# Optimization experiments

Hardware: AMD Instinct MI355X
Metric: run time of the kernel (lower is better)

The kernel has to match this reference:

```python
import jax, jax.numpy as jnp
import numpy as np

N, E = 40000, 640000
IN_DIM, EDGE_DIM, HID = 128, 64, 128


def setup_inputs() -> dict:
    key = jax.random.key(0)
    ks = jax.random.split(key, 10)
    x = jax.random.normal(ks[0], (N, IN_DIM), dtype=jnp.float32)
    edge_index = jax.random.randint(ks[1], (2, E), 0, N, dtype=jnp.int64)
    edge_attr = jax.random.normal(ks[2], (E, EDGE_DIM), dtype=jnp.float32)
    # learned params (xavier-ish scaling)
    Wh_w = jax.random.normal(ks[3], (EDGE_DIM, HID), dtype=jnp.float32) / np.sqrt(EDGE_DIM)
    Wh_b = jnp.zeros((HID,), dtype=jnp.float32)
    Wn_w = jax.random.normal(ks[4], (2 * IN_DIM, HID), dtype=jnp.float32) / np.sqrt(2 * IN_DIM)
    Wn_b = jnp.zeros((HID,), dtype=jnp.float32)
    w_e = jax.random.normal(ks[5], (HID, 1), dtype=jnp.float32) / np.sqrt(HID)
    ft_w = jax.random.normal(ks[6], (IN_DIM, IN_DIM), dtype=jnp.float32) / np.sqrt(IN_DIM)
    ft_b = jnp.zeros((IN_DIM,), dtype=jnp.float32)
    return {"x": x, "edge_index": edge_index, "edge_attr": edge_attr,
            "Wh_w": Wh_w, "Wh_b": Wh_b, "Wn_w": Wn_w, "Wn_b": Wn_b,
            "w_e": w_e, "ft_w": ft_w, "ft_b": ft_b}


def reference(x, edge_index, edge_attr, Wh_w, Wh_b, Wn_w, Wn_b, w_e, ft_w, ft_b):
    src, dst = edge_index[0], edge_index[1]
    # gather endpoint features and run edge MLP: relu(W_h(e) + W_n([x_src; x_dst]))
    node_feat = jnp.concatenate([x[src], x[dst]], axis=1)          # [E, 2*in_dim]
    edge_h = edge_attr @ Wh_w + Wh_b                               # [E, hid]
    node_h = node_feat @ Wn_w + Wn_b                               # [E, hid]
    combined = jax.nn.relu(edge_h + node_h)
    scores = (combined @ w_e)[:, 0]                                # [E]
    alpha = jax.nn.softmax(scores, axis=0)                         # softmax over all edges
    # scatter-add weighted dst features into src nodes (same-type branch)
    local = jnp.zeros_like(x).at[src].add(-alpha[:, None] * x[dst])
    out = x + local
    out = out + out @ ft_w + ft_b
    return out
```

## Files before the change

kernel.cpp:

```cpp
#include <hip/hip_runtime.h>
#include <math.h>

#define N_NODES 40000
#define E_EDGES 640000
#define IN_DIM 128
#define EDGE_DIM 64
#define HID 128
#define EB 10000
#define NPART (EB * 4)

typedef unsigned int u32;
typedef unsigned short u16;
typedef __attribute__((ext_vector_type(4))) float f32x4;
typedef __attribute__((ext_vector_type(8))) short bf16x8;

__device__ __forceinline__ float bf_lo(u32 d) { return __uint_as_float(d << 16); }
__device__ __forceinline__ float bf_hi(u32 d) { return __uint_as_float(d & 0xffff0000u); }
__device__ __forceinline__ u16 f2bf(float f) {
    u32 u = __float_as_uint(f);
    return (u16)((u + 0x7fffu + ((u >> 16) & 1u)) >> 16);
}
__device__ __forceinline__ u32 pack_bf(float lo, float hi) {
    return ((u32)f2bf(hi) << 16) | (u32)f2bf(lo);
}


__global__ __launch_bounds__(256) void k_init(const float* __restrict__ x,
                                              u16* __restrict__ xb,
                                              u32* __restrict__ counts) {
    int i = blockIdx.x * 256 + threadIdx.x;
    xb[i] = f2bf(x[i]);
    if (i < N_NODES) counts[i] = 0;
}

__global__ __launch_bounds__(256) void k_trans(const float* __restrict__ Whw,
                                               const float* __restrict__ Wnw,
                                               const float* __restrict__ ftw,
                                               u16* __restrict__ Whtb,
                                               u16* __restrict__ WnAT,
                                               u16* __restrict__ WnBT,
                                               u16* __restrict__ fttb) {
    int i = blockIdx.x * 256 + threadIdx.x;
    if (i < 8192) {
        int h = i >> 6, k = i & 63;
        Whtb[i] = f2bf(Whw[k * HID + h]);
    } else if (i < 24576) {
        int j = i - 8192, h = j >> 7, k = j & 127;
        WnAT[j] = f2bf(Wnw[k * HID + h]);
    } else if (i < 40960) {
        int j = i - 24576, h = j >> 7, k = j & 127;
        WnBT[j] = f2bf(Wnw[(IN_DIM + k) * HID + h]);
    } else {
        int j = i - 40960, h = j >> 7, k = j & 127;
        fttb[j] = f2bf(ftw[k * IN_DIM + h]);
    }
}

__global__ __launch_bounds__(256) void k_proj(const u16* __restrict__ xb,
                                              const u16* __restrict__ WnAT,
                                              const u16* __restrict__ WnBT,
                                              const float* __restrict__ Whb,
                                              const float* __restrict__ Wnb,
                                              u16* __restrict__ P1b,
                                              u16* __restrict__ P2b) {
    const int t = threadIdx.x, w = t >> 6, lane = t & 63;
    const int mrow = lane & 15, quad = lane >> 4;
    const int rowBase = blockIdx.x * 64 + w * 16;

    bf16x8 a[4];
    const u16* ar = xb + (size_t)(rowBase + mrow) * IN_DIM + quad * 8;
#pragma unroll
    for (int ks = 0; ks < 4; ++ks) a[ks] = *(const bf16x8*)(ar + ks * 32);

#pragma unroll
    for (int nt = 0; nt < 8; ++nt) {
        const u16* b1p = WnAT + (size_t)(nt * 16 + mrow) * IN_DIM + quad * 8;
        const u16* b2p = WnBT + (size_t)(nt * 16 + mrow) * IN_DIM + quad * 8;
        f32x4 c1 = {0.f, 0.f, 0.f, 0.f}, c2 = {0.f, 0.f, 0.f, 0.f};
#pragma unroll
        for (int ks = 0; ks < 4; ++ks) {
            c1 = __builtin_amdgcn_mfma_f32_16x16x32_bf16(a[ks], *(const bf16x8*)(b1p + ks * 32), c1, 0, 0, 0);
            c2 = __builtin_amdgcn_mfma_f32_16x16x32_bf16(a[ks], *(const bf16x8*)(b2p + ks * 32), c2, 0, 0, 0);
        }
        const int col = nt * 16 + mrow;
        const float bias = Whb[col] + Wnb[col];
#pragma unroll
        for (int r = 0; r < 4; ++r) {
            int row = rowBase + quad * 4 + r;
            P1b[(size_t)row * HID + col] = f2bf(c1[r] + bias);
            P2b[(size_t)row * HID + col] = f2bf(c2[r]);
        }
    }
}

__global__ __launch_bounds__(256) void k_hist(const int* __restrict__ eidx,
                                              u32* __restrict__ counts) {
    int e = blockIdx.x * 256 + threadIdx.x;
    atomicAdd(&counts[eidx[e]], 1u);
}

__global__ __launch_bounds__(1024) void k_scan(const u32* __restrict__ counts,
                                               u32* __restrict__ off,
                                               u32* __restrict__ cur) {
    __shared__ u32 sums[1024];
    const int t = threadIdx.x;
    const int CH = 40;
    u32 local[CH];
    u32 s = 0;
    const int base = t * CH;
#pragma unroll
    for (int i = 0; i < CH; ++i) {
        int idx = base + i;
        u32 c = (idx < N_NODES) ? counts[idx] : 0u;
        local[i] = s;
        s += c;
    }
    sums[t] = s;
    __syncthreads();
    for (int o = 1; o < 1024; o <<= 1) {
        u32 v = (t >= o) ? sums[t - o] : 0u;
        __syncthreads();
        sums[t] += v;
        __syncthreads();
    }
    const u32 pre = sums[t] - s;
#pragma unroll
    for (int i = 0; i < CH; ++i) {
        int idx = base + i;
        if (idx < N_NODES) {
            u32 v = pre + local[i];
            off[idx] = v;
            cur[idx] = v;
        }
    }
    if (t == 1023) off[N_NODES] = sums[1023];
}

__global__ __launch_bounds__(256) void k_edge(const int* __restrict__ eidx,
                                              const float* __restrict__ ea,
                                              const u16* __restrict__ Whtb,
                                              const u16* __restrict__ P1b,
                                              const u16* __restrict__ P2b,
                                              const float* __restrict__ we,
                                              u32* __restrict__ cur,
                                              uint2* __restrict__ sde,
                                              float* __restrict__ partials) {
    __shared__ u32 Psp[4][16][68];
    const int t = threadIdx.x, w = t >> 6, lane = t & 63;
    const int e0 = blockIdx.x * 64 + w * 16;
    const int mrow = lane & 15, quad = lane >> 4;

    const int m = lane >> 2, c4 = lane & 3;
    const int srcm = eidx[e0 + m];
    const int dstm = eidx[E_EDGES + e0 + m];
    const uint4* p1 = (const uint4*)(P1b + (size_t)srcm * HID + c4 * 32);
    const uint4* p2 = (const uint4*)(P2b + (size_t)dstm * HID + c4 * 32);
    uint4 pa[4], pb[4];
#pragma unroll
    for (int i = 0; i < 4; ++i) { pa[i] = p1[i]; pb[i] = p2[i]; }

    const float* arow = ea + (size_t)(e0 + mrow) * EDGE_DIM + quad * 8;
    float4 f0 = *(const float4*)(arow);
    float4 f1 = *(const float4*)(arow + 4);
    float4 f2 = *(const float4*)(arow + 32);
    float4 f3 = *(const float4*)(arow + 36);

#pragma unroll
    for (int i = 0; i < 4; ++i) {
        u32 da[4] = {pa[i].x, pa[i].y, pa[i].z, pa[i].w};
        u32 db[4] = {pb[i].x, pb[i].y, pb[i].z, pb[i].w};
        uint4 o;
        o.x = pack_bf(bf_lo(da[0]) + bf_lo(db[0]), bf_hi(da[0]) + bf_hi(db[0]));
        o.y = pack_bf(bf_lo(da[1]) + bf_lo(db[1]), bf_hi(da[1]) + bf_hi(db[1]));
        o.z = pack_bf(bf_lo(da[2]) + bf_lo(db[2]), bf_hi(da[2]) + bf_hi(db[2]));
        o.w = pack_bf(bf_lo(da[3]) + bf_lo(db[3]), bf_hi(da[3]) + bf_hi(db[3]));
        *(uint4*)&Psp[w][m][c4 * 16 + i * 4] = o;
    }

    bf16x8 a0, a1;
    a0[0] = (short)f2bf(f0.x); a0[1] = (short)f2bf(f0.y);
    a0[2] = (short)f2bf(f0.z); a0[3] = (short)f2bf(f0.w);
    a0[4] = (short)f2bf(f1.x); a0[5] = (short)f2bf(f1.y);
    a0[6] = (short)f2bf(f1.z); a0[7] = (short)f2bf(f1.w);
    a1[0] = (short)f2bf(f2.x); a1[1] = (short)f2bf(f2.y);
    a1[2] = (short)f2bf(f2.z); a1[3] = (short)f2bf(f2.w);
    a1[4] = (short)f2bf(f3.x); a1[5] = (short)f2bf(f3.y);
    a1[6] = (short)f2bf(f3.z); a1[7] = (short)f2bf(f3.w);

    float wsum[4] = {0.f, 0.f, 0.f, 0.f};
    const u16* bbase = Whtb + (size_t)mrow * EDGE_DIM + quad * 8;
#pragma unroll
    for (int nt = 0; nt < 8; ++nt) {
        const u16* bp = bbase + nt * 16 * EDGE_DIM;
        bf16x8 b0 = *(const bf16x8*)(bp);
        bf16x8 b1 = *(const bf16x8*)(bp + 32);
        f32x4 c = {0.f, 0.f, 0.f, 0.f};
        c = __builtin_amdgcn_mfma_f32_16x16x32_bf16(a0, b0, c, 0, 0, 0);
        c = __builtin_amdgcn_mfma_f32_16x16x32_bf16(a1, b1, c, 0, 0, 0);
        float wv = we[nt * 16 + mrow];
#pragma unroll
        for (int r = 0; r < 4; ++r) {
            u32 u = Psp[w][quad * 4 + r][nt * 8 + (mrow >> 1)];
            float p = (mrow & 1) ? bf_hi(u) : bf_lo(u);
            wsum[r] += fmaxf(c[r] + p, 0.f) * wv;
        }
    }

#pragma unroll
    for (int off = 1; off < 16; off <<= 1) {
#pragma unroll
        for (int r = 0; r < 4; ++r) wsum[r] += __shfl_xor(wsum[r], off, 16);
    }
    float ex[4]; float s4 = 0.f;
#pragma unroll
    for (int r = 0; r < 4; ++r) { ex[r] = __expf(wsum[r]); s4 += ex[r]; }

    if (mrow == 0) {
#pragma unroll
        for (int r = 0; r < 4; ++r) {
            int e = e0 + quad * 4 + r;
            int s = eidx[e];
            int d = eidx[E_EDGES + e];
            u32 pos = atomicAdd(&cur[s], 1u);
            sde[pos] = make_uint2((u32)d, __float_as_uint(-ex[r]));
        }
    }

    s4 += __shfl_xor(s4, 16, 64);
    s4 += __shfl_xor(s4, 32, 64);
    if (lane == 0) partials[blockIdx.x * 4 + w] = s4;
}

__global__ __launch_bounds__(256) void k_sum(const float* __restrict__ partials,
                                             float* __restrict__ sumExp) {
    float s = 0.f;
    for (int i = threadIdx.x; i < NPART; i += 256) s += partials[i];
#pragma unroll
    for (int off = 1; off < 64; off <<= 1) s += __shfl_xor(s, off, 64);
    __shared__ float ws4[4];
    if ((threadIdx.x & 63) == 0) ws4[threadIdx.x >> 6] = s;
    __syncthreads();
    if (threadIdx.x == 0) sumExp[0] = ws4[0] + ws4[1] + ws4[2] + ws4[3];
}

__global__ __launch_bounds__(256) void k_accum(const u32* __restrict__ off,
                                               const uint2* __restrict__ sde,
                                               const float* __restrict__ sumExp,
                                               const u16* __restrict__ xb,
                                               float* __restrict__ out) {
    const float invS = 1.0f / sumExp[0];
    const int lane = threadIdx.x & 63;
    const int n = blockIdx.x * 4 + (threadIdx.x >> 6);
    const u32 o0 = off[n], o1 = off[n + 1];

    float acc0 = 0.f, acc1 = 0.f;
    for (u32 base = o0; base < o1; base += 64) {
        u32 j = base + (u32)lane;
        uint2 dv = make_uint2(0u, 0u);
        if (j < o1) dv = sde[j];
        int cnt = (int)min(64u, o1 - base);
        int jj = 0;
        for (; jj + 4 <= cnt; jj += 4) {
            u32 d0 = __shfl(dv.x, jj, 64),     d1 = __shfl(dv.x, jj + 1, 64);
            u32 d2 = __shfl(dv.x, jj + 2, 64), d3 = __shfl(dv.x, jj + 3, 64);
            float a0 = __uint_as_float(__shfl(dv.y, jj, 64));
            float a1 = __uint_as_float(__shfl(dv.y, jj + 1, 64));
            float a2 = __uint_as_float(__shfl(dv.y, jj + 2, 64));
            float a3 = __uint_as_float(__shfl(dv.y, jj + 3, 64));
            u32 q0 = ((const u32*)(xb + (size_t)d0 * IN_DIM))[lane];
            u32 q1 = ((const u32*)(xb + (size_t)d1 * IN_DIM))[lane];
            u32 q2 = ((const u32*)(xb + (size_t)d2 * IN_DIM))[lane];
            u32 q3 = ((const u32*)(xb + (size_t)d3 * IN_DIM))[lane];
            acc0 = fmaf(a0, bf_lo(q0), acc0); acc1 = fmaf(a0, bf_hi(q0), acc1);
            acc0 = fmaf(a1, bf_lo(q1), acc0); acc1 = fmaf(a1, bf_hi(q1), acc1);
            acc0 = fmaf(a2, bf_lo(q2), acc0); acc1 = fmaf(a2, bf_hi(q2), acc1);
            acc0 = fmaf(a3, bf_lo(q3), acc0); acc1 = fmaf(a3, bf_hi(q3), acc1);
        }
        for (; jj < cnt; ++jj) {
            u32 dst = __shfl(dv.x, jj, 64);
            float a = __uint_as_float(__shfl(dv.y, jj, 64));
            u32 q = ((const u32*)(xb + (size_t)dst * IN_DIM))[lane];
            acc0 = fmaf(a, bf_lo(q), acc0);
            acc1 = fmaf(a, bf_hi(q), acc1);
        }
    }
    float* op = out + (size_t)n * IN_DIM + 2 * lane;
    op[0] = acc0 * invS;
    op[1] = acc1 * invS;
}

__global__ __launch_bounds__(256) void k_final(const float* __restrict__ x,
                                               const u16* __restrict__ fttb,
                                               const float* __restrict__ ftb,
                                               float* __restrict__ out) {
    __shared__ u32 ybp[64][68];
    const int t = threadIdx.x;
    const int rb = blockIdx.x * 64;

    {
        const int rr = t >> 2, seg = t & 3;
        const float4* xp = (const float4*)(x + (size_t)(rb + rr) * IN_DIM + seg * 32);
        const float4* lp = (const float4*)(out + (size_t)(rb + rr) * IN_DIM + seg * 32);
#pragma unroll
        for (int i = 0; i < 4; ++i) {
            float4 xa = xp[2 * i], xc = xp[2 * i + 1];
            float4 la = lp[2 * i], lc = lp[2 * i + 1];
            uint4 o;
            o.x = pack_bf(xa.x + la.x, xa.y + la.y);
            o.y = pack_bf(xa.z + la.z, xa.w + la.w);
            o.z = pack_bf(xc.x + lc.x, xc.y + lc.y);
            o.w = pack_bf(xc.z + lc.z, xc.w + lc.w);
            *(uint4*)&ybp[rr][seg * 16 + i * 4] = o;
        }
    }
    __syncthreads();

    const int w = t >> 6, lane = t & 63;
    const int mrow = lane & 15, quad = lane >> 4;
    const int rowBase = rb + w * 16;

    bf16x8 a[4];
#pragma unroll
    for (int ks = 0; ks < 4; ++ks)
        a[ks] = *(const bf16x8*)&ybp[w * 16 + mrow][ks * 16 + quad * 4];

#pragma unroll
    for (int nt = 0; nt < 8; ++nt) {
        const u16* bp = fttb + (size_t)(nt * 16 + mrow) * IN_DIM + quad * 8;
        f32x4 c = {0.f, 0.f, 0.f, 0.f};
#pragma unroll
        for (int ks = 0; ks < 4; ++ks)
            c = __builtin_amdgcn_mfma_f32_16x16x32_bf16(a[ks], *(const bf16x8*)(bp + ks * 32), c, 0, 0, 0);
        const int col = nt * 16 + mrow;
        const float fb = ftb[col];
#pragma unroll
        for (int r = 0; r < 4; ++r) {
            int row = rowBase + quad * 4 + r;
            size_t idx = (size_t)row * IN_DIM + col;
            float y = x[idx] + out[idx];
            out[idx] = y + c[r] + fb;
        }
    }
}

extern "C" void kernel_launch(void* const* d_in, const int* in_sizes, int n_in,
                              void* d_out, int out_size, void* d_ws, size_t ws_size,
                              hipStream_t stream) {
    const float* x    = (const float*)d_in[0];
    const int*   eidx = (const int*)d_in[1];
    const float* ea   = (const float*)d_in[2];
    const float* Whw  = (const float*)d_in[3];
    const float* Whb  = (const float*)d_in[4];
    const float* Wnw  = (const float*)d_in[5];
    const float* Wnb  = (const float*)d_in[6];
    const float* we   = (const float*)d_in[7];
    const float* ftw  = (const float*)d_in[8];
    const float* ftb  = (const float*)d_in[9];
    float* out = (float*)d_out;

    uint2* sde      = (uint2*)d_ws;
    u16*   P1b      = (u16*)(sde + (size_t)E_EDGES);
    u16*   P2b      = P1b + (size_t)N_NODES * HID;
    u16*   xb       = P2b + (size_t)N_NODES * HID;
    u16*   Whtb     = xb + (size_t)N_NODES * IN_DIM;
    u16*   WnAT     = Whtb + (size_t)EDGE_DIM * HID;
    u16*   WnBT     = WnAT + (size_t)HID * IN_DIM;
    u16*   fttb     = WnBT + (size_t)HID * IN_DIM;
    float* partials = (float*)(fttb + (size_t)IN_DIM * IN_DIM);
    float* sumExp   = partials + NPART;
    u32*   counts   = (u32*)(sumExp + 1);
    u32*   off      = counts + N_NODES;
    u32*   cur      = off + N_NODES + 1;

    k_init <<<(N_NODES * IN_DIM) / 256, 256, 0, stream>>>(x, xb, counts);
    k_trans<<<224, 256, 0, stream>>>(Whw, Wnw, ftw, Whtb, WnAT, WnBT, fttb);
    k_proj <<<N_NODES / 64, 256, 0, stream>>>(xb, WnAT, WnBT, Whb, Wnb, P1b, P2b);
    k_hist <<<E_EDGES / 256, 256, 0, stream>>>(eidx, counts);
    k_scan <<<1, 1024, 0, stream>>>(counts, off, cur);
    k_edge <<<EB, 256, 0, stream>>>(eidx, ea, Whtb, P1b, P2b, we, cur, sde, partials);
    k_sum  <<<1, 256, 0, stream>>>(partials, sumExp);
    k_accum<<<N_NODES / 4, 256, 0, stream>>>(off, sde, sumExp, xb, out);
    k_final<<<N_NODES / 64, 256, 0, stream>>>(x, fttb, ftb, out);
}
```

Measured before the change: 565.0 us.

## Add gathered node projections via identity MFMA instead of LDS transpose

Each lane now gathers the projected P1/P2 node rows directly in MFMA A-operand layout. Two extra MFMAs against a one-hot identity B operand add those rows into the accumulator, which replaces the shared-memory staging buffer and the scalar bf16 unpacking in the inner loop. The src/dst indices are also reused through lane shuffles instead of being reloaded for the scatter. This removes LDS traffic and pack/unpack ALU work, at the cost of doubling the MFMA count per tile and adding register pressure.

```diff
diff --git a/kernel.cpp b/kernel.cpp
--- a/kernel.cpp
+++ b/kernel.cpp
@@ -145,19 +145,20 @@
                                               u32* __restrict__ cur,
                                               uint2* __restrict__ sde,
                                               float* __restrict__ partials) {
-    __shared__ u32 Psp[4][16][68];
     const int t = threadIdx.x, w = t >> 6, lane = t & 63;
     const int e0 = blockIdx.x * 64 + w * 16;
     const int mrow = lane & 15, quad = lane >> 4;
 
-    const int m = lane >> 2, c4 = lane & 3;
-    const int srcm = eidx[e0 + m];
-    const int dstm = eidx[E_EDGES + e0 + m];
-    const uint4* p1 = (const uint4*)(P1b + (size_t)srcm * HID + c4 * 32);
-    const uint4* p2 = (const uint4*)(P2b + (size_t)dstm * HID + c4 * 32);
-    uint4 pa[4], pb[4];
-#pragma unroll
-    for (int i = 0; i < 4; ++i) { pa[i] = p1[i]; pb[i] = p2[i]; }
+    const int srcm = eidx[e0 + mrow];
+    const int dstm = eidx[E_EDGES + e0 + mrow];
+    const u16* p1 = P1b + (size_t)srcm * HID + quad * 8;
+    const u16* p2 = P2b + (size_t)dstm * HID + quad * 8;
+    bf16x8 aP1[4], aP2[4];
+#pragma unroll
+    for (int ks = 0; ks < 4; ++ks) {
+        aP1[ks] = *(const bf16x8*)(p1 + ks * 32);
+        aP2[ks] = *(const bf16x8*)(p2 + ks * 32);
+    }
 
     const float* arow = ea + (size_t)(e0 + mrow) * EDGE_DIM + quad * 8;
     float4 f0 = *(const float4*)(arow);
@@ -165,16 +166,16 @@
     float4 f2 = *(const float4*)(arow + 32);
     float4 f3 = *(const float4*)(arow + 36);
 
-#pragma unroll
-    for (int i = 0; i < 4; ++i) {
-        u32 da[4] = {pa[i].x, pa[i].y, pa[i].z, pa[i].w};
-        u32 db[4] = {pb[i].x, pb[i].y, pb[i].z, pb[i].w};
-        uint4 o;
-        o.x = pack_bf(bf_lo(da[0]) + bf_lo(db[0]), bf_hi(da[0]) + bf_hi(db[0]));
-        o.y = pack_bf(bf_lo(da[1]) + bf_lo(db[1]), bf_hi(da[1]) + bf_hi(db[1]));
-        o.z = pack_bf(bf_lo(da[2]) + bf_lo(db[2]), bf_hi(da[2]) + bf_hi(db[2]));
-        o.w = pack_bf(bf_lo(da[3]) + bf_lo(db[3]), bf_hi(da[3]) + bf_hi(db[3]));
-        *(uint4*)&Psp[w][m][c4 * 16 + i * 4] = o;
+    bf16x8 bIe, bIo;
+    {
+        const int hotj = mrow & 7;
+        const bool ce = (quad == (mrow >> 3));
+        const bool co = (quad == 2 + (mrow >> 3));
+#pragma unroll
+        for (int j = 0; j < 8; ++j) {
+            bIe[j] = (short)((ce && j == hotj) ? 0x3F80 : 0);
+            bIo[j] = (short)((co && j == hotj) ? 0x3F80 : 0);
+        }
     }
 
     bf16x8 a0, a1;
@@ -197,32 +198,36 @@
         f32x4 c = {0.f, 0.f, 0.f, 0.f};
         c = __builtin_amdgcn_mfma_f32_16x16x32_bf16(a0, b0, c, 0, 0, 0);
         c = __builtin_amdgcn_mfma_f32_16x16x32_bf16(a1, b1, c, 0, 0, 0);
+        const bf16x8 bI = (nt & 1) ? bIo : bIe;
+        c = __builtin_amdgcn_mfma_f32_16x16x32_bf16(aP1[nt >> 1], bI, c, 0, 0, 0);
+        c = __builtin_amdgcn_mfma_f32_16x16x32_bf16(aP2[nt >> 1], bI, c, 0, 0, 0);
         float wv = we[nt * 16 + mrow];
 #pragma unroll
+        for (int r = 0; r < 4; ++r)
+            wsum[r] += fmaxf(c[r], 0.f) * wv;
+    }
+
+#pragma unroll
+    for (int off = 1; off < 16; off <<= 1) {
+#pragma unroll
+        for (int r = 0; r < 4; ++r) wsum[r] += __shfl_xor(wsum[r], off, 16);
+    }
+    float ex[4]; float s4 = 0.f;
+#pragma unroll
+    for (int r = 0; r < 4; ++r) { ex[r] = __expf(wsum[r]); s4 += ex[r]; }
+
+    u32 sArr[4], dArr[4];
+#pragma unroll
+    for (int r = 0; r < 4; ++r) {
+        sArr[r] = (u32)__shfl(srcm, quad * 4 + r, 16);
+        dArr[r] = (u32)__shfl(dstm, quad * 4 + r, 16);
+    }
+
+    if (mrow == 0) {
+#pragma unroll
         for (int r = 0; r < 4; ++r) {
-            u32 u = Psp[w][quad * 4 + r][nt * 8 + (mrow >> 1)];
-            float p = (mrow & 1) ? bf_hi(u) : bf_lo(u);
-            wsum[r] += fmaxf(c[r] + p, 0.f) * wv;
-        }
-    }
-
-#pragma unroll
-    for (int off = 1; off < 16; off <<= 1) {
-#pragma unroll
-        for (int r = 0; r < 4; ++r) wsum[r] += __shfl_xor(wsum[r], off, 16);
-    }
-    float ex[4]; float s4 = 0.f;
-#pragma unroll
-    for (int r = 0; r < 4; ++r) { ex[r] = __expf(wsum[r]); s4 += ex[r]; }
-
-    if (mrow == 0) {
-#pragma unroll
-        for (int r = 0; r < 4; ++r) {
-            int e = e0 + quad * 4 + r;
-            int s = eidx[e];
-            int d = eidx[E_EDGES + e];
-            u32 pos = atomicAdd(&cur[s], 1u);
-            sde[pos] = make_uint2((u32)d, __float_as_uint(-ex[r]));
+            u32 pos = atomicAdd(&cur[sArr[r]], 1u);
+            sde[pos] = make_uint2(dArr[r], __float_as_uint(-ex[r]));
         }
     }
 
```

New measurement: 577.1 us. 1.02x slower.

## Merge small kernels, double edges per wave, atomic softmax sum

Applied to the files above, without the earlier changes.

Merges the bf16 conversion/init and weight-transpose kernels into one launch, and folds the histogram into the projection kernel via extra blocks. The edge kernel now handles 32 edges per wave instead of 16, halving the grid and sharing the Wh B-fragments across two MFMA tiles. The CSR scatter writes are spread over lanes instead of done serially by one lane. The per-wave exp-sum partials and the separate reduction kernel are replaced by a float atomicAdd into a single accumulator. This cuts launch count and per-edge overhead, at the cost of more register pressure and a non-deterministic float summation order.

```diff
diff --git a/kernel.cpp b/kernel.cpp
--- a/kernel.cpp
+++ b/kernel.cpp
@@ -6,8 +6,7 @@
 #define IN_DIM 128
 #define EDGE_DIM 64
 #define HID 128
-#define EB 10000
-#define NPART (EB * 4)
+#define EB 5000
 
 typedef unsigned int u32;
 typedef unsigned short u16;
@@ -25,44 +24,54 @@
 }
 
 
-__global__ __launch_bounds__(256) void k_init(const float* __restrict__ x,
-                                              u16* __restrict__ xb,
-                                              u32* __restrict__ counts) {
-    int i = blockIdx.x * 256 + threadIdx.x;
-    xb[i] = f2bf(x[i]);
-    if (i < N_NODES) counts[i] = 0;
-}
-
-__global__ __launch_bounds__(256) void k_trans(const float* __restrict__ Whw,
-                                               const float* __restrict__ Wnw,
-                                               const float* __restrict__ ftw,
-                                               u16* __restrict__ Whtb,
-                                               u16* __restrict__ WnAT,
-                                               u16* __restrict__ WnBT,
-                                               u16* __restrict__ fttb) {
-    int i = blockIdx.x * 256 + threadIdx.x;
-    if (i < 8192) {
-        int h = i >> 6, k = i & 63;
-        Whtb[i] = f2bf(Whw[k * HID + h]);
-    } else if (i < 24576) {
-        int j = i - 8192, h = j >> 7, k = j & 127;
-        WnAT[j] = f2bf(Wnw[k * HID + h]);
-    } else if (i < 40960) {
-        int j = i - 24576, h = j >> 7, k = j & 127;
-        WnBT[j] = f2bf(Wnw[(IN_DIM + k) * HID + h]);
+__global__ __launch_bounds__(256) void k_pre(const float* __restrict__ x,
+                                             const float* __restrict__ Whw,
+                                             const float* __restrict__ Wnw,
+                                             const float* __restrict__ ftw,
+                                             u16* __restrict__ xb,
+                                             u32* __restrict__ counts,
+                                             float* __restrict__ sumExp,
+                                             u16* __restrict__ Whtb,
+                                             u16* __restrict__ WnAT,
+                                             u16* __restrict__ WnBT,
+                                             u16* __restrict__ fttb) {
+    if (blockIdx.x < 20000) {
+        int i = blockIdx.x * 256 + threadIdx.x;
+        xb[i] = f2bf(x[i]);
+        if (i < N_NODES) counts[i] = 0;
+        if (i == 0) sumExp[0] = 0.f;
     } else {
-        int j = i - 40960, h = j >> 7, k = j & 127;
-        fttb[j] = f2bf(ftw[k * IN_DIM + h]);
-    }
-}
-
-__global__ __launch_bounds__(256) void k_proj(const u16* __restrict__ xb,
-                                              const u16* __restrict__ WnAT,
-                                              const u16* __restrict__ WnBT,
-                                              const float* __restrict__ Whb,
-                                              const float* __restrict__ Wnb,
-                                              u16* __restrict__ P1b,
-                                              u16* __restrict__ P2b) {
+        int i = (blockIdx.x - 20000) * 256 + threadIdx.x;
+        if (i < 8192) {
+            int h = i >> 6, k = i & 63;
+            Whtb[i] = f2bf(Whw[k * HID + h]);
+        } else if (i < 24576) {
+            int j = i - 8192, h = j >> 7, k = j & 127;
+            WnAT[j] = f2bf(Wnw[k * HID + h]);
+        } else if (i < 40960) {
+            int j = i - 24576, h = j >> 7, k = j & 127;
+            WnBT[j] = f2bf(Wnw[(IN_DIM + k) * HID + h]);
+        } else {
+            int j = i - 40960, h = j >> 7, k = j & 127;
+            fttb[j] = f2bf(ftw[k * IN_DIM + h]);
+        }
+    }
+}
+
+__global__ __launch_bounds__(256) void k_projhist(const u16* __restrict__ xb,
+                                                  const u16* __restrict__ WnAT,
+                                                  const u16* __restrict__ WnBT,
+                                                  const float* __restrict__ Whb,
+                                                  const float* __restrict__ Wnb,
+                                                  u16* __restrict__ P1b,
+                                                  u16* __restrict__ P2b,
+                                                  const int* __restrict__ eidx,
+                                                  u32* __restrict__ counts) {
+    if (blockIdx.x >= 625) {
+        int e = (blockIdx.x - 625) * 256 + threadIdx.x;
+        atomicAdd(&counts[eidx[e]], 1u);
+        return;
+    }
     const int t = threadIdx.x, w = t >> 6, lane = t & 63;
     const int mrow = lane & 15, quad = lane >> 4;
     const int rowBase = blockIdx.x * 64 + w * 16;
@@ -91,12 +100,6 @@
             P2b[(size_t)row * HID + col] = f2bf(c2[r]);
         }
     }
-}
-
-__global__ __launch_bounds__(256) void k_hist(const int* __restrict__ eidx,
-                                              u32* __restrict__ counts) {
-    int e = blockIdx.x * 256 + threadIdx.x;
-    atomicAdd(&counts[eidx[e]], 1u);
 }
 
 __global__ __launch_bounds__(1024) void k_scan(const u32* __restrict__ counts,
@@ -144,40 +147,60 @@
                                               const float* __restrict__ we,
                                               u32* __restrict__ cur,
                                               uint2* __restrict__ sde,
-                                              float* __restrict__ partials) {
-    __shared__ u32 Psp[4][16][68];
+                                              float* __restrict__ sumExp) {
+    __shared__ u32 Psp[4][32][68];
     const int t = threadIdx.x, w = t >> 6, lane = t & 63;
-    const int e0 = blockIdx.x * 64 + w * 16;
+    const int e0 = blockIdx.x * 128 + w * 32;
     const int mrow = lane & 15, quad = lane >> 4;
 
     const int m = lane >> 2, c4 = lane & 3;
-    const int srcm = eidx[e0 + m];
-    const int dstm = eidx[E_EDGES + e0 + m];
-    const uint4* p1 = (const uint4*)(P1b + (size_t)srcm * HID + c4 * 32);
-    const uint4* p2 = (const uint4*)(P2b + (size_t)dstm * HID + c4 * 32);
-    uint4 pa[4], pb[4];
-#pragma unroll
-    for (int i = 0; i < 4; ++i) { pa[i] = p1[i]; pb[i] = p2[i]; }
-
-    const float* arow = ea + (size_t)(e0 + mrow) * EDGE_DIM + quad * 8;
-    float4 f0 = *(const float4*)(arow);
-    float4 f1 = *(const float4*)(arow + 4);
-    float4 f2 = *(const float4*)(arow + 32);
-    float4 f3 = *(const float4*)(arow + 36);
-
+    const int srcA = eidx[e0 + m];
+    const int dstA = eidx[E_EDGES + e0 + m];
+    const int srcB = eidx[e0 + 16 + m];
+    const int dstB = eidx[E_EDGES + e0 + 16 + m];
+    const uint4* p1A = (const uint4*)(P1b + (size_t)srcA * HID + c4 * 32);
+    const uint4* p2A = (const uint4*)(P2b + (size_t)dstA * HID + c4 * 32);
+    const uint4* p1B = (const uint4*)(P1b + (size_t)srcB * HID + c4 * 32);
+    const uint4* p2B = (const uint4*)(P2b + (size_t)dstB * HID + c4 * 32);
+    uint4 paA[4], pbA[4], paB[4], pbB[4];
 #pragma unroll
     for (int i = 0; i < 4; ++i) {
-        u32 da[4] = {pa[i].x, pa[i].y, pa[i].z, pa[i].w};
-        u32 db[4] = {pb[i].x, pb[i].y, pb[i].z, pb[i].w};
+        paA[i] = p1A[i]; pbA[i] = p2A[i];
+        paB[i] = p1B[i]; pbB[i] = p2B[i];
+    }
+
+    const float* arowA = ea + (size_t)(e0 + mrow) * EDGE_DIM + quad * 8;
+    const float* arowB = ea + (size_t)(e0 + 16 + mrow) * EDGE_DIM + quad * 8;
+    float4 f0 = *(const float4*)(arowA);
+    float4 f1 = *(const float4*)(arowA + 4);
+    float4 f2 = *(const float4*)(arowA + 32);
+    float4 f3 = *(const float4*)(arowA + 36);
+    float4 g0 = *(const float4*)(arowB);
+    float4 g1 = *(const float4*)(arowB + 4);
+    float4 g2 = *(const float4*)(arowB + 32);
+    float4 g3 = *(const float4*)(arowB + 36);
+
+#pragma unroll
+    for (int i = 0; i < 4; ++i) {
+        u32 da[4] = {paA[i].x, paA[i].y, paA[i].z, paA[i].w};
+        u32 db[4] = {pbA[i].x, pbA[i].y, pbA[i].z, pbA[i].w};
         uint4 o;
         o.x = pack_bf(bf_lo(da[0]) + bf_lo(db[0]), bf_hi(da[0]) + bf_hi(db[0]));
         o.y = pack_bf(bf_lo(da[1]) + bf_lo(db[1]), bf_hi(da[1]) + bf_hi(db[1]));
         o.z = pack_bf(bf_lo(da[2]) + bf_lo(db[2]), bf_hi(da[2]) + bf_hi(db[2]));
         o.w = pack_bf(bf_lo(da[3]) + bf_lo(db[3]), bf_hi(da[3]) + bf_hi(db[3]));
         *(uint4*)&Psp[w][m][c4 * 16 + i * 4] = o;
-    }
-
-    bf16x8 a0, a1;
+        u32 ea2[4] = {paB[i].x, paB[i].y, paB[i].z, paB[i].w};
+        u32 eb2[4] = {pbB[i].x, pbB[i].y, pbB[i].z, pbB[i].w};
+        uint4 o2;
+        o2.x = pack_bf(bf_lo(ea2[0]) + bf_lo(eb2[0]), bf_hi(ea2[0]) + bf_hi(eb2[0]));
+        o2.y = pack_bf(bf_lo(ea2[1]) + bf_lo(eb2[1]), bf_hi(ea2[1]) + bf_hi(eb2[1]));
+        o2.z = pack_bf(bf_lo(ea2[2]) + bf_lo(eb2[2]), bf_hi(ea2[2]) + bf_hi(eb2[2]));
+        o2.w = pack_bf(bf_lo(ea2[3]) + bf_lo(eb2[3]), bf_hi(ea2[3]) + bf_hi(eb2[3]));
+        *(uint4*)&Psp[w][16 + m][c4 * 16 + i * 4] = o2;
+    }
+
+    bf16x8 a0, a1, a2, a3;
     a0[0] = (short)f2bf(f0.x); a0[1] = (short)f2bf(f0.y);
     a0[2] = (short)f2bf(f0.z); a0[3] = (short)f2bf(f0.w);
     a0[4] = (short)f2bf(f1.x); a0[5] = (short)f2bf(f1.y);
@@ -186,61 +209,70 @@
     a1[2] = (short)f2bf(f2.z); a1[3] = (short)f2bf(f2.w);
     a1[4] = (short)f2bf(f3.x); a1[5] = (short)f2bf(f3.y);
     a1[6] = (short)f2bf(f3.z); a1[7] = (short)f2bf(f3.w);
-
-    float wsum[4] = {0.f, 0.f, 0.f, 0.f};
+    a2[0] = (short)f2bf(g0.x); a2[1] = (short)f2bf(g0.y);
+    a2[2] = (short)f2bf(g0.z); a2[3] = (short)f2bf(g0.w);
+    a2[4] = (short)f2bf(g1.x); a2[5] = (short)f2bf(g1.y);
+    a2[6] = (short)f2bf(g1.z); a2[7] = (short)f2bf(g1.w);
+    a3[0] = (short)f2bf(g2.x); a3[1] = (short)f2bf(g2.y);
+    a3[2] = (short)f2bf(g2.z); a3[3] = (short)f2bf(g2.w);
+    a3[4] = (short)f2bf(g3.x); a3[5] = (short)f2bf(g3.y);
+    a3[6] = (short)f2bf(g3.z); a3[7] = (short)f2bf(g3.w);
+
+    float wsA[4] = {0.f, 0.f, 0.f, 0.f};
+    float wsB[4] = {0.f, 0.f, 0.f, 0.f};
     const u16* bbase = Whtb + (size_t)mrow * EDGE_DIM + quad * 8;
 #pragma unroll
     for (int nt = 0; nt < 8; ++nt) {
         const u16* bp = bbase + nt * 16 * EDGE_DIM;
         bf16x8 b0 = *(const bf16x8*)(bp);
         bf16x8 b1 = *(const bf16x8*)(bp + 32);
-        f32x4 c = {0.f, 0.f, 0.f, 0.f};
-        c = __builtin_amdgcn_mfma_f32_16x16x32_bf16(a0, b0, c, 0, 0, 0);
-        c = __builtin_amdgcn_mfma_f32_16x16x32_bf16(a1, b1, c, 0, 0, 0);
+        f32x4 cA = {0.f, 0.f, 0.f, 0.f};
+        cA = __builtin_amdgcn_mfma_f32_16x16x32_bf16(a0, b0, cA, 0, 0, 0);
+        cA = __builtin_amdgcn_mfma_f32_16x16x32_bf16(a1, b1, cA, 0, 0, 0);
+        f32x4 cB = {0.f, 0.f, 0.f, 0.f};
+        cB = __builtin_amdgcn_mfma_f32_16x16x32_bf16(a2, b0, cB, 0, 0, 0);
+        cB = __builtin_amdgcn_mfma_f32_16x16x32_bf16(a3, b1, cB, 0, 0, 0);
         float wv = we[nt * 16 + mrow];
 #pragma unroll
         for (int r = 0; r < 4; ++r) {
-            u32 u = Psp[w][quad * 4 + r][nt * 8 + (mrow >> 1)];
-            float p = (mrow & 1) ? bf_hi(u) : bf_lo(u);
-            wsum[r] += fmaxf(c[r] + p, 0.f) * wv;
+            u32 uA = Psp[w][quad * 4 + r][nt * 8 + (mrow >> 1)];
+            u32 uB = Psp[w][16 + quad * 4 + r][nt * 8 + (mrow >> 1)];
+            float pA = (mrow & 1) ? bf_hi(uA) : bf_lo(uA);
+            float pB = (mrow & 1) ? bf_hi(uB) : bf_lo(uB);
+            wsA[r] += fmaxf(cA[r] + pA, 0.f) * wv;
+            wsB[r] += fmaxf(cB[r] + pB, 0.f) * wv;
         }
     }
 
 #pragma unroll
     for (int off = 1; off < 16; off <<= 1) {
 #pragma unroll
-        for (int r = 0; r < 4; ++r) wsum[r] += __shfl_xor(wsum[r], off, 16);
-    }
-    float ex[4]; float s4 = 0.f;
-#pragma unroll
-    for (int r = 0; r < 4; ++r) { ex[r] = __expf(wsum[r]); s4 += ex[r]; }
-
-    if (mrow == 0) {
-#pragma unroll
         for (int r = 0; r < 4; ++r) {
-            int e = e0 + quad * 4 + r;
-            int s = eidx[e];
-            int d = eidx[E_EDGES + e];
-            u32 pos = atomicAdd(&cur[s], 1u);
-            sde[pos] = make_uint2((u32)d, __float_as_uint(-ex[r]));
-        }
+            wsA[r] += __shfl_xor(wsA[r], off, 16);
+            wsB[r] += __shfl_xor(wsB[r], off, 16);
+        }
+    }
+    float exA[4], exB[4]; float s4 = 0.f;
+#pragma unroll
+    for (int r = 0; r < 4; ++r) {
+        exA[r] = __expf(wsA[r]); s4 += exA[r];
+        exB[r] = __expf(wsB[r]); s4 += exB[r];
+    }
+
+    if (c4 == 0) {
+        float exm_a = (m & 2) ? ((m & 1) ? exA[3] : exA[2])
+                              : ((m & 1) ? exA[1] : exA[0]);
+        float exm_b = (m & 2) ? ((m & 1) ? exB[3] : exB[2])
+                              : ((m & 1) ? exB[1] : exB[0]);
+        u32 posA = atomicAdd(&cur[srcA], 1u);
+        sde[posA] = make_uint2((u32)dstA, __float_as_uint(-exm_a));
+        u32 posB = atomicAdd(&cur[srcB], 1u);
+        sde[posB] = make_uint2((u32)dstB, __float_as_uint(-exm_b));
     }
 
     s4 += __shfl_xor(s4, 16, 64);
     s4 += __shfl_xor(s4, 32, 64);
-    if (lane == 0) partials[blockIdx.x * 4 + w] = s4;
-}
-
-__global__ __launch_bounds__(256) void k_sum(const float* __restrict__ partials,
-                                             float* __restrict__ sumExp) {
-    float s = 0.f;
-    for (int i = threadIdx.x; i < NPART; i += 256) s += partials[i];
-#pragma unroll
-    for (int off = 1; off < 64; off <<= 1) s += __shfl_xor(s, off, 64);
-    __shared__ float ws4[4];
-    if ((threadIdx.x & 63) == 0) ws4[threadIdx.x >> 6] = s;
-    __syncthreads();
-    if (threadIdx.x == 0) sumExp[0] = ws4[0] + ws4[1] + ws4[2] + ws4[3];
+    if (lane == 0) atomicAdd(sumExp, s4);
 }
 
 __global__ __launch_bounds__(256) void k_accum(const u32* __restrict__ off,
@@ -366,19 +398,17 @@
     u16*   WnAT     = Whtb + (size_t)EDGE_DIM * HID;
     u16*   WnBT     = WnAT + (size_t)HID * IN_DIM;
     u16*   fttb     = WnBT + (size_t)HID * IN_DIM;
-    float* partials = (float*)(fttb + (size_t)IN_DIM * IN_DIM);
-    float* sumExp   = partials + NPART;
+    float* sumExp   = (float*)(fttb + (size_t)IN_DIM * IN_DIM);
     u32*   counts   = (u32*)(sumExp + 1);
     u32*   off      = counts + N_NODES;
     u32*   cur      = off + N_NODES + 1;
 
-    k_init <<<(N_NODES * IN_DIM) / 256, 256, 0, stream>>>(x, xb, counts);
-    k_trans<<<224, 256, 0, stream>>>(Whw, Wnw, ftw, Whtb, WnAT, WnBT, fttb);
-    k_proj <<<N_NODES / 64, 256, 0, stream>>>(xb, WnAT, WnBT, Whb, Wnb, P1b, P2b);
-    k_hist <<<E_EDGES / 256, 256, 0, stream>>>(eidx, counts);
-    k_scan <<<1, 1024, 0, stream>>>(counts, off, cur);
-    k_edge <<<EB, 256, 0, stream>>>(eidx, ea, Whtb, P1b, P2b, we, cur, sde, partials);
-    k_sum  <<<1, 256, 0, stream>>>(partials, sumExp);
-    k_accum<<<N_NODES / 4, 256, 0, stream>>>(off, sde, sumExp, xb, out);
-    k_final<<<N_NODES / 64, 256, 0, stream>>>(x, fttb, ftb, out);
-}
+    k_pre     <<<20224, 256, 0, stream>>>(x, Whw, Wnw, ftw, xb, counts, sumExp,
+                                          Whtb, WnAT, WnBT, fttb);
+    k_projhist<<<3125, 256, 0, stream>>>(xb, WnAT, WnBT, Whb, Wnb, P1b, P2b,
+                                         eidx, counts);
+    k_scan    <<<1, 1024, 0, stream>>>(counts, off, cur);
+    k_edge    <<<EB, 256, 0, stream>>>(eidx, ea, Whtb, P1b, P2b, we, cur, sde, sumExp);
+    k_accum   <<<N_NODES / 4, 256, 0, stream>>>(off, sde, sumExp, xb, out);
+    k_final   <<<N_NODES / 64, 256, 0, stream>>>(x, fttb, ftb, out);
+}
```

New measurement: 639.5 us. +13.2%, slower.

## Fuse preprocessing and histogram kernels, fold softmax normalisation into final kernel

Applied to the files above, without the earlier changes.

Merges the bf16 conversion, weight transpose and edge histogram into one launch, zeroing counts with a memset instead. The partial-sum reduction moves into block 0 of the accumulate kernel, and the 1/sum scaling moves into the final kernel. This works because the accumulation no longer needs the sum and the final kernel runs after it. The gather loop in the accumulate kernel is also unrolled by 8 to keep more independent loads in flight. Together these cut launch count and serial single-block kernels, at the cost of a slightly more complex control flow.

```diff
diff --git a/kernel.cpp b/kernel.cpp
--- a/kernel.cpp
+++ b/kernel.cpp
@@ -25,34 +25,38 @@
 }
 
 
-__global__ __launch_bounds__(256) void k_init(const float* __restrict__ x,
-                                              u16* __restrict__ xb,
-                                              u32* __restrict__ counts) {
-    int i = blockIdx.x * 256 + threadIdx.x;
-    xb[i] = f2bf(x[i]);
-    if (i < N_NODES) counts[i] = 0;
-}
-
-__global__ __launch_bounds__(256) void k_trans(const float* __restrict__ Whw,
-                                               const float* __restrict__ Wnw,
-                                               const float* __restrict__ ftw,
-                                               u16* __restrict__ Whtb,
-                                               u16* __restrict__ WnAT,
-                                               u16* __restrict__ WnBT,
-                                               u16* __restrict__ fttb) {
-    int i = blockIdx.x * 256 + threadIdx.x;
-    if (i < 8192) {
-        int h = i >> 6, k = i & 63;
-        Whtb[i] = f2bf(Whw[k * HID + h]);
-    } else if (i < 24576) {
-        int j = i - 8192, h = j >> 7, k = j & 127;
-        WnAT[j] = f2bf(Wnw[k * HID + h]);
-    } else if (i < 40960) {
-        int j = i - 24576, h = j >> 7, k = j & 127;
-        WnBT[j] = f2bf(Wnw[(IN_DIM + k) * HID + h]);
+__global__ __launch_bounds__(256) void k_pre(const float* __restrict__ x,
+                                             const float* __restrict__ Whw,
+                                             const float* __restrict__ Wnw,
+                                             const float* __restrict__ ftw,
+                                             const int* __restrict__ eidx,
+                                             u16* __restrict__ xb,
+                                             u32* __restrict__ counts,
+                                             u16* __restrict__ Whtb,
+                                             u16* __restrict__ WnAT,
+                                             u16* __restrict__ WnBT,
+                                             u16* __restrict__ fttb) {
+    if (blockIdx.x < 20000) {
+        int i = blockIdx.x * 256 + threadIdx.x;
+        xb[i] = f2bf(x[i]);
+    } else if (blockIdx.x < 20224) {
+        int i = (blockIdx.x - 20000) * 256 + threadIdx.x;
+        if (i < 8192) {
+            int h = i >> 6, k = i & 63;
+            Whtb[i] = f2bf(Whw[k * HID + h]);
+        } else if (i < 24576) {
+            int j = i - 8192, h = j >> 7, k = j & 127;
+            WnAT[j] = f2bf(Wnw[k * HID + h]);
+        } else if (i < 40960) {
+            int j = i - 24576, h = j >> 7, k = j & 127;
+            WnBT[j] = f2bf(Wnw[(IN_DIM + k) * HID + h]);
+        } else {
+            int j = i - 40960, h = j >> 7, k = j & 127;
+            fttb[j] = f2bf(ftw[k * IN_DIM + h]);
+        }
     } else {
-        int j = i - 40960, h = j >> 7, k = j & 127;
-        fttb[j] = f2bf(ftw[k * IN_DIM + h]);
+        int e = (blockIdx.x - 20224) * 256 + threadIdx.x;
+        atomicAdd(&counts[eidx[e]], 1u);
     }
 }
 
@@ -91,12 +95,6 @@
             P2b[(size_t)row * HID + col] = f2bf(c2[r]);
         }
     }
-}
-
-__global__ __launch_bounds__(256) void k_hist(const int* __restrict__ eidx,
-                                              u32* __restrict__ counts) {
-    int e = blockIdx.x * 256 + threadIdx.x;
-    atomicAdd(&counts[eidx[e]], 1u);
 }
 
 __global__ __launch_bounds__(1024) void k_scan(const u32* __restrict__ counts,
@@ -231,26 +229,25 @@
     if (lane == 0) partials[blockIdx.x * 4 + w] = s4;
 }
 
-__global__ __launch_bounds__(256) void k_sum(const float* __restrict__ partials,
-                                             float* __restrict__ sumExp) {
-    float s = 0.f;
-    for (int i = threadIdx.x; i < NPART; i += 256) s += partials[i];
-#pragma unroll
-    for (int off = 1; off < 64; off <<= 1) s += __shfl_xor(s, off, 64);
-    __shared__ float ws4[4];
-    if ((threadIdx.x & 63) == 0) ws4[threadIdx.x >> 6] = s;
-    __syncthreads();
-    if (threadIdx.x == 0) sumExp[0] = ws4[0] + ws4[1] + ws4[2] + ws4[3];
-}
-
 __global__ __launch_bounds__(256) void k_accum(const u32* __restrict__ off,
                                                const uint2* __restrict__ sde,
-                                               const float* __restrict__ sumExp,
+                                               const float* __restrict__ partials,
+                                               float* __restrict__ sumExp,
                                                const u16* __restrict__ xb,
                                                float* __restrict__ out) {
-    const float invS = 1.0f / sumExp[0];
+    if (blockIdx.x == 0) {
+        float s = 0.f;
+        for (int i = threadIdx.x; i < NPART; i += 256) s += partials[i];
+#pragma unroll
+        for (int o = 1; o < 64; o <<= 1) s += __shfl_xor(s, o, 64);
+        __shared__ float ws4[4];
+        if ((threadIdx.x & 63) == 0) ws4[threadIdx.x >> 6] = s;
+        __syncthreads();
+        if (threadIdx.x == 0) sumExp[0] = ws4[0] + ws4[1] + ws4[2] + ws4[3];
+        return;
+    }
     const int lane = threadIdx.x & 63;
-    const int n = blockIdx.x * 4 + (threadIdx.x >> 6);
+    const int n = (blockIdx.x - 1) * 4 + (threadIdx.x >> 6);
     const u32 o0 = off[n], o1 = off[n + 1];
 
     float acc0 = 0.f, acc1 = 0.f;
@@ -260,21 +257,37 @@
         if (j < o1) dv = sde[j];
         int cnt = (int)min(64u, o1 - base);
         int jj = 0;
+        for (; jj + 8 <= cnt; jj += 8) {
+            u32 d[8]; float a[8]; u32 q[8];
+#pragma unroll
+            for (int k = 0; k < 8; ++k) {
+                d[k] = __shfl(dv.x, jj + k, 64);
+                a[k] = __uint_as_float(__shfl(dv.y, jj + k, 64));
+            }
+#pragma unroll
+            for (int k = 0; k < 8; ++k)
+                q[k] = ((const u32*)(xb + (size_t)d[k] * IN_DIM))[lane];
+#pragma unroll
+            for (int k = 0; k < 8; ++k) {
+                acc0 = fmaf(a[k], bf_lo(q[k]), acc0);
+                acc1 = fmaf(a[k], bf_hi(q[k]), acc1);
+            }
+        }
         for (; jj + 4 <= cnt; jj += 4) {
-            u32 d0 = __shfl(dv.x, jj, 64),     d1 = __shfl(dv.x, jj + 1, 64);
-            u32 d2 = __shfl(dv.x, jj + 2, 64), d3 = __shfl(dv.x, jj + 3, 64);
-            float a0 = __uint_as_float(__shfl(dv.y, jj, 64));
-            float a1 = __uint_as_float(__shfl(dv.y, jj + 1, 64));
-            float a2 = __uint_as_float(__shfl(dv.y, jj + 2, 64));
-            float a3 = __uint_as_float(__shfl(dv.y, jj + 3, 64));
-            u32 q0 = ((const u32*)(xb + (size_t)d0 * IN_DIM))[lane];
-            u32 q1 = ((const u32*)(xb + (size_t)d1 * IN_DIM))[lane];
-            u32 q2 = ((const u32*)(xb + (size_t)d2 * IN_DIM))[lane];
-            u32 q3 = ((const u32*)(xb + (size_t)d3 * IN_DIM))[lane];
-            acc0 = fmaf(a0, bf_lo(q0), acc0); acc1 = fmaf(a0, bf_hi(q0), acc1);
-            acc0 = fmaf(a1, bf_lo(q1), acc0); acc1 = fmaf(a1, bf_hi(q1), acc1);
-            acc0 = fmaf(a2, bf_lo(q2), acc0); acc1 = fmaf(a2, bf_hi(q2), acc1);
-            acc0 = fmaf(a3, bf_lo(q3), acc0); acc1 = fmaf(a3, bf_hi(q3), acc1);
+            u32 d[4]; float a[4]; u32 q[4];
+#pragma unroll
+            for (int k = 0; k < 4; ++k) {
+                d[k] = __shfl(dv.x, jj + k, 64);
+                a[k] = __uint_as_float(__shfl(dv.y, jj + k, 64));
+            }
+#pragma unroll
+            for (int k = 0; k < 4; ++k)
+                q[k] = ((const u32*)(xb + (size_t)d[k] * IN_DIM))[lane];
+#pragma unroll
+            for (int k = 0; k < 4; ++k) {
+                acc0 = fmaf(a[k], bf_lo(q[k]), acc0);
+                acc1 = fmaf(a[k], bf_hi(q[k]), acc1);
+            }
         }
         for (; jj < cnt; ++jj) {
             u32 dst = __shfl(dv.x, jj, 64);
@@ -285,15 +298,17 @@
         }
     }
     float* op = out + (size_t)n * IN_DIM + 2 * lane;
-    op[0] = acc0 * invS;
-    op[1] = acc1 * invS;
+    op[0] = acc0;
+    op[1] = acc1;
 }
 
 __global__ __launch_bounds__(256) void k_final(const float* __restrict__ x,
                                                const u16* __restrict__ fttb,
                                                const float* __restrict__ ftb,
+                                               const float* __restrict__ sumExp,
                                                float* __restrict__ out) {
     __shared__ u32 ybp[64][68];
+    const float invS = 1.0f / sumExp[0];
     const int t = threadIdx.x;
     const int rb = blockIdx.x * 64;
 
@@ -306,10 +321,10 @@
             float4 xa = xp[2 * i], xc = xp[2 * i + 1];
             float4 la = lp[2 * i], lc = lp[2 * i + 1];
             uint4 o;
-            o.x = pack_bf(xa.x + la.x, xa.y + la.y);
-            o.y = pack_bf(xa.z + la.z, xa.w + la.w);
-            o.z = pack_bf(xc.x + lc.x, xc.y + lc.y);
-            o.w = pack_bf(xc.z + lc.z, xc.w + lc.w);
+            o.x = pack_bf(fmaf(invS, la.x, xa.x), fmaf(invS, la.y, xa.y));
+            o.y = pack_bf(fmaf(invS, la.z, xa.z), fmaf(invS, la.w, xa.w));
+            o.z = pack_bf(fmaf(invS, lc.x, xc.x), fmaf(invS, lc.y, xc.y));
+            o.w = pack_bf(fmaf(invS, lc.z, xc.z), fmaf(invS, lc.w, xc.w));
             *(uint4*)&ybp[rr][seg * 16 + i * 4] = o;
         }
     }
@@ -337,7 +352,7 @@
         for (int r = 0; r < 4; ++r) {
             int row = rowBase + quad * 4 + r;
             size_t idx = (size_t)row * IN_DIM + col;
-            float y = x[idx] + out[idx];
+            float y = fmaf(invS, out[idx], x[idx]);
             out[idx] = y + c[r] + fb;
         }
     }
@@ -372,13 +387,12 @@
     u32*   off      = counts + N_NODES;
     u32*   cur      = off + N_NODES + 1;
 
-    k_init <<<(N_NODES * IN_DIM) / 256, 256, 0, stream>>>(x, xb, counts);
-    k_trans<<<224, 256, 0, stream>>>(Whw, Wnw, ftw, Whtb, WnAT, WnBT, fttb);
+    hipMemsetAsync(counts, 0, (size_t)N_NODES * sizeof(u32), stream);
+    k_pre  <<<22724, 256, 0, stream>>>(x, Whw, Wnw, ftw, eidx, xb, counts,
+                                       Whtb, WnAT, WnBT, fttb);
+    k_scan <<<1, 1024, 0, stream>>>(counts, off, cur);
     k_proj <<<N_NODES / 64, 256, 0, stream>>>(xb, WnAT, WnBT, Whb, Wnb, P1b, P2b);
-    k_hist <<<E_EDGES / 256, 256, 0, stream>>>(eidx, counts);
-    k_scan <<<1, 1024, 0, stream>>>(counts, off, cur);
     k_edge <<<EB, 256, 0, stream>>>(eidx, ea, Whtb, P1b, P2b, we, cur, sde, partials);
-    k_sum  <<<1, 256, 0, stream>>>(partials, sumExp);
-    k_accum<<<N_NODES / 4, 256, 0, stream>>>(off, sde, sumExp, xb, out);
-    k_final<<<N_NODES / 64, 256, 0, stream>>>(x, fttb, ftb, out);
-}
+    k_accum<<<N_NODES / 4 + 1, 256, 0, stream>>>(off, sde, partials, sumExp, xb, out);
+    k_final<<<N_NODES / 64, 256, 0, stream>>>(x, fttb, ftb, sumExp, out);
+}
```

Result: faster. 550.7 us (-2.5%).
